# Optimization experiments

Measured on AMD Instinct MI355X. Metric: run time of the kernel, lower is better.

## Reference

```python
import jax, jax.numpy as jnp
import numpy as np

B, IN_DIM, HIDDEN, OUT_DIM = 256, 100000, 512, 30000
KS, DIM = 256, 2
S = HIDDEN // DIM  # number of PQ subspaces = 256


def setup_inputs() -> dict:
    key = jax.random.key(0)
    ks = jax.random.split(key, 6)
    x = jax.random.uniform(ks[0], (B, IN_DIM), dtype=jnp.float32)
    w1 = jax.random.normal(ks[1], (HIDDEN, IN_DIM), dtype=jnp.float32) * 0.01
    b1 = jax.random.normal(ks[2], (HIDDEN,), dtype=jnp.float32)
    codebooks = jax.random.normal(ks[3], (S, KS, DIM), dtype=jnp.float32) * 0.05
    codes = jax.random.randint(ks[4], (OUT_DIM, S), 0, KS, dtype=jnp.int64)
    b2 = jax.random.normal(ks[5], (OUT_DIM,), dtype=jnp.float32) * 0.01
    return {"x": x, "w1": w1, "b1": b1, "codebooks": codebooks,
            "codes": codes, "b2": b2}


def reference(x, w1, b1, codebooks, codes, b2):
    # fc1: SparseLinear == x @ w1.T + b1 (spmm with dense math)
    h = jax.nn.relu(jnp.einsum('bi,hi->bh', x, w1) + b1)  # [B, HIDDEN]
    # fc2: VQLinear -- reconstruct PQ weight via codebook gather
    # codebooks: [S, KS, DIM], codes: [OUT_DIM, S] -> w2: [OUT_DIM, S, DIM]
    w2 = codebooks[jnp.arange(S)[None, :], codes]            # gather per subspace
    w2 = w2.reshape(OUT_DIM, HIDDEN)                         # [OUT_DIM, HIDDEN]
    logits = jnp.einsum('bh,oh->bo', h, w2) + b2             # [B, OUT_DIM]
    # original applies log_softmax over dim=0 (batch axis)
    return jax.nn.log_softmax(logits, axis=0)
```

## Files before the change

### kernel.cpp

```cpp
#include <hip/hip_runtime.h>
#include <cstdint>
#include <cstddef>

#define B_ 256
#define IN_ 100000
#define H_ 512
#define OUT_ 30000
#define OUTP_ 30080
#define S_ 256
#define NSTEPS 3125
#define KSPLIT 64

typedef __attribute__((ext_vector_type(4))) float f32x4;
typedef __attribute__((ext_vector_type(2))) float f32x2;
typedef __attribute__((ext_vector_type(4))) int i32x4;
typedef __attribute__((ext_vector_type(8))) short short8;
typedef __attribute__((ext_vector_type(8))) unsigned short ushort8;
typedef __attribute__((ext_vector_type(4))) unsigned short ushort4_;
typedef __attribute__((ext_vector_type(2))) uint32_t uint32x2;
typedef __attribute__((ext_vector_type(4))) uint32_t uint32x4;

static __device__ __forceinline__ uint32_t cvtpk(float lo, float hi) {
  uint32_t r;
  asm("v_cvt_pk_bf16_f32 %0, %1, %2" : "=v"(r) : "v"(lo), "v"(hi));
  return r;
}
static __device__ __forceinline__ unsigned short f2bf(float f) {
  union { float f; uint32_t u; } c; c.f = f;
  uint32_t u = c.u;
  u += 0x7FFFu + ((u >> 16) & 1u);
  return (unsigned short)(u >> 16);
}
static __device__ __forceinline__ float bf2f(unsigned short h) {
  union { uint32_t u; float f; } c; c.u = ((uint32_t)h) << 16;
  return c.f;
}
static __device__ __forceinline__ void pack4_store(unsigned short* dst, f32x4 a) {
  uint32x2 v;
  v[0] = cvtpk(a[0], a[1]); v[1] = cvtpk(a[2], a[3]);
  *(uint32x2*)dst = v;
}

#define BARRIER() { asm volatile("s_waitcnt lgkmcnt(0)" ::: "memory"); \
    __builtin_amdgcn_s_barrier(); \
    __builtin_amdgcn_sched_barrier(0); }

__global__ __launch_bounds__(512, 2) void k_gemm1(const float* __restrict__ x,
                                                  const float* __restrict__ w1,
                                                  unsigned short* __restrict__ part) {
  __shared__ alignas(16) unsigned short Ab[2][B_ * 32];
  __shared__ alignas(16) unsigned short Bb[2][128 * 32];
  const int tid = threadIdx.x;
  const int d = blockIdx.x;
  const int xcd = d & 7;
  const int i = d >> 3;
  const int kc = xcd + ((i >> 2) << 3);
  const int nblk = i & 3;
  const int s0 = (kc * NSTEPS) / KSPLIT;
  const int s1 = ((kc + 1) * NSTEPS) / KSPLIT;
  const int U = s1 - s0;

  const int arow = tid >> 3;
  const int asl = tid & 7;
  const size_t rowStride64 = (size_t)64 * IN_;
  const float* gA = x + (size_t)arow * IN_ + (size_t)s0 * 32 + asl * 4;
  const int afz = (arow >> 1) & 3;
  const int aslSw = ((asl >> 1) ^ afz) * 8 + (asl & 1) * 4;

  const int br = tid >> 3;
  const int bj = tid & 7;
  const float* gB = w1 + (size_t)(nblk * 128 + br) * IN_ + (size_t)s0 * 32 + bj * 4;
  const int bOff = br * 32 + (((bj >> 1) ^ ((br >> 1) & 3)) * 8) + (bj & 1) * 4;

  const int lane = tid & 63;
  const int wid = tid >> 6;
  const int wrow = wid >> 1;
  const int wcol = wid & 1;
  const int fr = lane & 15;
  const int fq = lane >> 4;
  const int Ra = wrow * 64 + fr;
  const int Rb = wcol * 64 + fr;
  const int aBase = Ra * 32 + (fq ^ ((Ra >> 1) & 3)) * 8;
  const int bBase = Rb * 32 + (fq ^ ((Rb >> 1) & 3)) * 8;

  f32x4 zero = {0.f, 0.f, 0.f, 0.f};
  f32x4 acc[4][4];
  #pragma unroll
  for (int mf = 0; mf < 4; ++mf)
    #pragma unroll
    for (int nf = 0; nf < 4; ++nf) acc[mf][nf] = zero;

  f32x4 P0, P1, P2, P3, P4, P5;
  f32x4 Q0, Q1, Q2, Q3, Q4, Q5;
  f32x4 R0, R1, R2, R3, R4, R5;
  f32x4 S0, S1, S2, S3, S4, S5;

#define G1_ISSUE(S, u) if ((u) < U) { \
    const float* pa_ = gA + (size_t)(u) * 32; \
    S##0 = *(const f32x4*)pa_; \
    S##1 = *(const f32x4*)(pa_ + rowStride64); \
    S##2 = *(const f32x4*)(pa_ + 2 * rowStride64); \
    S##3 = *(const f32x4*)(pa_ + 3 * rowStride64); \
    const float* pb_ = gB + (size_t)(u) * 32; \
    S##4 = *(const f32x4*)pb_; \
    S##5 = *(const f32x4*)(pb_ + rowStride64); }

#define G1_PACK(S, b) { \
    pack4_store(&Ab[b][(arow)       * 32 + aslSw], S##0); \
    pack4_store(&Ab[b][(arow + 64)  * 32 + aslSw], S##1); \
    pack4_store(&Ab[b][(arow + 128) * 32 + aslSw], S##2); \
    pack4_store(&Ab[b][(arow + 192) * 32 + aslSw], S##3); \
    pack4_store(&Bb[b][bOff], S##4); \
    pack4_store(&Bb[b][bOff + 64 * 32], S##5); }

#define COMPUTE_TILE(b) { \
    short8 af_[4], bf_[4]; \
    _Pragma("unroll") for (int mf_ = 0; mf_ < 4; ++mf_) af_[mf_] = *(const short8*)&Ab[b][aBase + mf_ * 512]; \
    _Pragma("unroll") for (int nf_ = 0; nf_ < 4; ++nf_) bf_[nf_] = *(const short8*)&Bb[b][bBase + nf_ * 512]; \
    __builtin_amdgcn_s_setprio(1); \
    _Pragma("unroll") for (int mf_ = 0; mf_ < 4; ++mf_) \
      _Pragma("unroll") for (int nf_ = 0; nf_ < 4; ++nf_) \
        acc[mf_][nf_] = __builtin_amdgcn_mfma_f32_16x16x32_bf16(af_[mf_], bf_[nf_], acc[mf_][nf_], 0, 0, 0); \
    __builtin_amdgcn_s_setprio(0); }

  G1_ISSUE(P, 0)
  G1_ISSUE(Q, 1)
  G1_ISSUE(R, 2)
  G1_ISSUE(S, 3)
  G1_PACK(P, 0)
  BARRIER()

  int u = 0;
  #pragma unroll 1
  while (u + 3 < U) {
    G1_ISSUE(P, u + 4)
    COMPUTE_TILE(0)
    G1_PACK(Q, 1)
    BARRIER()
    G1_ISSUE(Q, u + 5)
    COMPUTE_TILE(1)
    G1_PACK(R, 0)
    BARRIER()
    G1_ISSUE(R, u + 6)
    COMPUTE_TILE(0)
    G1_PACK(S, 1)
    BARRIER()
    G1_ISSUE(S, u + 7)
    COMPUTE_TILE(1)
    if (u + 4 < U) { G1_PACK(P, 0) }
    BARRIER()
    u += 4;
  }
  if (u < U)     COMPUTE_TILE(0)
  if (u + 1 < U) { G1_PACK(Q, 1) BARRIER() COMPUTE_TILE(1) }
  if (u + 2 < U) { G1_PACK(R, 0) BARRIER() COMPUTE_TILE(0) }
  if (u + 3 < U) { G1_PACK(S, 1) BARRIER() COMPUTE_TILE(1) }

  unsigned short* pp = part + (size_t)kc * (B_ * H_);
  #pragma unroll
  for (int mf = 0; mf < 4; ++mf) {
    #pragma unroll
    for (int nf = 0; nf < 4; ++nf) {
      const int row0 = wrow * 64 + mf * 16 + fq * 4;
      const int col = nblk * 128 + wcol * 64 + nf * 16 + fr;
      #pragma unroll
      for (int j = 0; j < 4; ++j)
        pp[(size_t)(row0 + j) * H_ + col] = f2bf(acc[mf][nf][j]);
    }
  }
}

__global__ void k_reduce_h(const unsigned short* __restrict__ part,
                           const float* __restrict__ b1,
                           unsigned short* __restrict__ hbf) {
  int t = blockIdx.x * 256 + threadIdx.x;
  int base = t * 4;
  int n = base & (H_ - 1);
  float a0 = b1[n], a1 = b1[n + 1], a2 = b1[n + 2], a3 = b1[n + 3];
  #pragma unroll 8
  for (int kc = 0; kc < KSPLIT; ++kc) {
    ushort4_ v = *(const ushort4_*)(part + (size_t)kc * (B_ * H_) + base);
    a0 += bf2f(v[0]); a1 += bf2f(v[1]); a2 += bf2f(v[2]); a3 += bf2f(v[3]);
  }
  ushort4_ o;
  o[0] = f2bf(fmaxf(a0, 0.f));
  o[1] = f2bf(fmaxf(a1, 0.f));
  o[2] = f2bf(fmaxf(a2, 0.f));
  o[3] = f2bf(fmaxf(a3, 0.f));
  *(ushort4_*)(hbf + base) = o;
}

__global__ __launch_bounds__(512, 2) void k_gemm2(const unsigned short* __restrict__ hbf,
                                                  const int* __restrict__ codes,
                                                  const float* __restrict__ cb,
                                                  const float* __restrict__ b2,
                                                  float* __restrict__ out) {
  __shared__ alignas(16) unsigned short Ab[2][B_ * 32];
  __shared__ alignas(16) unsigned short Bb[2][128 * 32];
  __shared__ float sred[4][128];
  const int tid = threadIdx.x;
  const int n0 = blockIdx.x * 128;

  const int arow2 = tid >> 2;
  const int asl2 = tid & 3;
  const unsigned short* gA = hbf + (size_t)arow2 * H_ + asl2 * 8;
  const int afz2 = (arow2 >> 1) & 3;
  const int aslSw2 = (asl2 ^ afz2) * 8;
  const int aOffA = arow2 * 32 + aslSw2;
  const int aOffB = (arow2 + 128) * 32 + aslSw2;

  const int rb = tid >> 2;
  const int s4 = tid & 3;
  const int rbo = (n0 + rb < OUT_) ? (n0 + rb) : (OUT_ - 1);
  const int* gC = codes + (size_t)rbo * S_ + s4 * 4;
  const int bOff = rb * 32 + (s4 ^ ((rb >> 1) & 3)) * 8;

  const int lane = tid & 63;
  const int wid = tid >> 6;
  const int wrow = wid >> 1;
  const int wcol = wid & 1;
  const int fr = lane & 15;
  const int fq = lane >> 4;
  const int Ra = wrow * 64 + fr;
  const int Rb = wcol * 64 + fr;
  const int aBase = Ra * 32 + (fq ^ ((Ra >> 1) & 3)) * 8;
  const int bBase = Rb * 32 + (fq ^ ((Rb >> 1) & 3)) * 8;

  f32x4 zero = {0.f, 0.f, 0.f, 0.f};
  f32x4 acc[4][4];
  #pragma unroll
  for (int mf = 0; mf < 4; ++mf)
    #pragma unroll
    for (int nf = 0; nf < 4; ++nf) acc[mf][nf] = zero;

  ushort8 Pa0, Pa1, Qa0, Qa1;
  i32x4 Pc, Qc;
  f32x2 Pg0, Pg1, Pg2, Pg3, Qg0, Qg1, Qg2, Qg3;

#define G2_IC(S, u) if ((u) < 16) { \
    S##a0 = *(const ushort8*)(gA + (size_t)(u) * 32); \
    S##a1 = *(const ushort8*)(gA + (size_t)(u) * 32 + (size_t)128 * H_); \
    S##c  = *(const i32x4*)(gC + (u) * 16); }

#define G2_IG(S, u) if ((u) < 16) { \
    const int slb_ = (u) * 16 + s4 * 4; \
    S##g0 = *(const f32x2*)(cb + ((size_t)(slb_ + 0) * 256 + (S##c[0] & 255)) * 2); \
    S##g1 = *(const f32x2*)(cb + ((size_t)(slb_ + 1) * 256 + (S##c[1] & 255)) * 2); \
    S##g2 = *(const f32x2*)(cb + ((size_t)(slb_ + 2) * 256 + (S##c[2] & 255)) * 2); \
    S##g3 = *(const f32x2*)(cb + ((size_t)(slb_ + 3) * 256 + (S##c[3] & 255)) * 2); }

#define G2_PACK(S, b) { \
    *(ushort8*)&Ab[b][aOffA] = S##a0; \
    *(ushort8*)&Ab[b][aOffB] = S##a1; \
    uint32x4 bw_; \
    bw_[0] = cvtpk(S##g0[0], S##g0[1]); bw_[1] = cvtpk(S##g1[0], S##g1[1]); \
    bw_[2] = cvtpk(S##g2[0], S##g2[1]); bw_[3] = cvtpk(S##g3[0], S##g3[1]); \
    *(uint32x4*)&Bb[b][bOff] = bw_; }

#define G2_COMPUTE(b) { \
    short8 af_[4], bf_[4]; \
    _Pragma("unroll") for (int mf_ = 0; mf_ < 4; ++mf_) af_[mf_] = *(const short8*)&Ab[b][aBase + mf_ * 512]; \
    _Pragma("unroll") for (int nf_ = 0; nf_ < 4; ++nf_) bf_[nf_] = *(const short8*)&Bb[b][bBase + nf_ * 512]; \
    __builtin_amdgcn_s_setprio(1); \
    _Pragma("unroll") for (int mf_ = 0; mf_ < 4; ++mf_) \
      _Pragma("unroll") for (int nf_ = 0; nf_ < 4; ++nf_) \
        acc[mf_][nf_] = __builtin_amdgcn_mfma_f32_16x16x32_bf16(af_[mf_], bf_[nf_], acc[mf_][nf_], 0, 0, 0); \
    __builtin_amdgcn_s_setprio(0); }

  G2_IC(P, 0)
  G2_IC(Q, 1)
  G2_IG(P, 0)
  G2_PACK(P, 0)
  BARRIER()

  #pragma unroll 1
  for (int u = 0; u < 16; u += 2) {
    G2_IC(P, u + 2)
    G2_IG(Q, u + 1)
    G2_COMPUTE(0)
    G2_PACK(Q, 1)
    BARRIER()
    G2_IC(Q, u + 3)
    G2_IG(P, u + 2)
    G2_COMPUTE(1)
    if (u + 2 < 16) { G2_PACK(P, 0) }
    BARRIER()
  }

  float b2v[4];
  #pragma unroll
  for (int nf = 0; nf < 4; ++nf) {
    int col = n0 + wcol * 64 + nf * 16 + fr;
    b2v[nf] = (col < OUT_) ? b2[col] : 0.f;
  }
  #pragma unroll
  for (int mf = 0; mf < 4; ++mf)
    #pragma unroll
    for (int nf = 0; nf < 4; ++nf)
      #pragma unroll
      for (int j = 0; j < 4; ++j) acc[mf][nf][j] += b2v[nf];

  float cmax[4];
  #pragma unroll
  for (int nf = 0; nf < 4; ++nf) {
    float m = -3.4e38f;
    #pragma unroll
    for (int mf = 0; mf < 4; ++mf)
      #pragma unroll
      for (int j = 0; j < 4; ++j) m = fmaxf(m, acc[mf][nf][j]);
    m = fmaxf(m, __shfl_xor(m, 16, 64));
    m = fmaxf(m, __shfl_xor(m, 32, 64));
    cmax[nf] = m;
  }
  if (lane < 16) {
    #pragma unroll
    for (int nf = 0; nf < 4; ++nf) sred[wrow][wcol * 64 + nf * 16 + lane] = cmax[nf];
  }
  __syncthreads();
  float cm[4];
  #pragma unroll
  for (int nf = 0; nf < 4; ++nf) {
    int ci = wcol * 64 + nf * 16 + fr;
    cm[nf] = fmaxf(fmaxf(sred[0][ci], sred[1][ci]), fmaxf(sred[2][ci], sred[3][ci]));
  }
  __syncthreads();

  float cs[4];
  #pragma unroll
  for (int nf = 0; nf < 4; ++nf) {
    float sum = 0.f;
    #pragma unroll
    for (int mf = 0; mf < 4; ++mf)
      #pragma unroll
      for (int j = 0; j < 4; ++j) sum += expf(acc[mf][nf][j] - cm[nf]);
    sum += __shfl_xor(sum, 16, 64);
    sum += __shfl_xor(sum, 32, 64);
    cs[nf] = sum;
  }
  if (lane < 16) {
    #pragma unroll
    for (int nf = 0; nf < 4; ++nf) sred[wrow][wcol * 64 + nf * 16 + lane] = cs[nf];
  }
  __syncthreads();
  float lden[4];
  #pragma unroll
  for (int nf = 0; nf < 4; ++nf) {
    int ci = wcol * 64 + nf * 16 + fr;
    lden[nf] = logf(sred[0][ci] + sred[1][ci] + sred[2][ci] + sred[3][ci]);
  }

  #pragma unroll
  for (int mf = 0; mf < 4; ++mf) {
    #pragma unroll
    for (int nf = 0; nf < 4; ++nf) {
      int col = n0 + wcol * 64 + nf * 16 + fr;
      if (col < OUT_) {
        int row0 = wrow * 64 + mf * 16 + fq * 4;
        #pragma unroll
        for (int j = 0; j < 4; ++j)
          out[(size_t)(row0 + j) * OUT_ + col] = acc[mf][nf][j] - cm[nf] - lden[nf];
      }
    }
  }
}

extern "C" void kernel_launch(void* const* d_in, const int* in_sizes, int n_in,
                              void* d_out, int out_size, void* d_ws, size_t ws_size,
                              hipStream_t stream) {
  const float* x      = (const float*)d_in[0];
  const float* w1     = (const float*)d_in[1];
  const float* b1     = (const float*)d_in[2];
  const float* cb     = (const float*)d_in[3];
  const int*   codes  = (const int*)d_in[4];
  const float* b2     = (const float*)d_in[5];
  float* out = (float*)d_out;

  char* ws = (char*)d_ws;
  unsigned short* part = (unsigned short*)ws;
  unsigned short* hbf  = (unsigned short*)(ws + (size_t)KSPLIT * B_ * H_ * 2);

  hipLaunchKernelGGL(k_gemm1,    dim3(4 * KSPLIT),          dim3(512), 0, stream, x, w1, part);
  hipLaunchKernelGGL(k_reduce_h, dim3((B_ * H_ / 4) / 256), dim3(256), 0, stream, part, b1, hbf);
  hipLaunchKernelGGL(k_gemm2,    dim3(OUTP_ / 128),         dim3(512), 0, stream, hbf, codes, cb, b2, out);
}
```

Before: 120.4 us.

## Stream fp32 tiles directly into LDS via global_load_lds triple buffering

Replaces the register-staged load, bf16 pack and LDS store pipeline in the first GEMM with direct global-to-LDS DMA (global_load_lds, 16 bytes per lane) into a three-stage fp32 LDS ring. The bf16 conversion moves to the LDS read side just before the MFMAs. The aim is to free VGPRs and VALU work from staging and to overlap loads with compute using a vmcnt-based wait. In exchange LDS footprint doubles per stage (fp32, three buffers, about 144KB), which may limit occupancy at two blocks per CU, and each tile now needs twice the LDS read traffic plus conversion work per compute step.

```diff
diff --git a/kernel.cpp b/kernel.cpp
--- a/kernel.cpp
+++ b/kernel.cpp
@@ -20,6 +20,8 @@
 typedef __attribute__((ext_vector_type(2))) uint32_t uint32x2;
 typedef __attribute__((ext_vector_type(4))) uint32_t uint32x4;
 
+union U32S8 { uint32x4 u; short8 s; };
+
 static __device__ __forceinline__ uint32_t cvtpk(float lo, float hi) {
   uint32_t r;
   asm("v_cvt_pk_bf16_f32 %0, %1, %2" : "=v"(r) : "v"(lo), "v"(hi));
@@ -35,21 +37,25 @@
   union { uint32_t u; float f; } c; c.u = ((uint32_t)h) << 16;
   return c.f;
 }
-static __device__ __forceinline__ void pack4_store(unsigned short* dst, f32x4 a) {
-  uint32x2 v;
-  v[0] = cvtpk(a[0], a[1]); v[1] = cvtpk(a[2], a[3]);
-  *(uint32x2*)dst = v;
+
+static __device__ __forceinline__ void gload_lds16(const float* g, float* l) {
+  __builtin_amdgcn_global_load_lds((const __attribute__((address_space(1))) void*)g,
+                                   (__attribute__((address_space(3))) void*)l, 16, 0, 0);
 }
 
 #define BARRIER() { asm volatile("s_waitcnt lgkmcnt(0)" ::: "memory"); \
     __builtin_amdgcn_s_barrier(); \
     __builtin_amdgcn_sched_barrier(0); }
 
+#define WAITBAR() { asm volatile("s_waitcnt vmcnt(6) lgkmcnt(0)" ::: "memory"); \
+    __builtin_amdgcn_s_barrier(); \
+    __builtin_amdgcn_sched_barrier(0); }
+
 __global__ __launch_bounds__(512, 2) void k_gemm1(const float* __restrict__ x,
                                                   const float* __restrict__ w1,
                                                   unsigned short* __restrict__ part) {
-  __shared__ alignas(16) unsigned short Ab[2][B_ * 32];
-  __shared__ alignas(16) unsigned short Bb[2][128 * 32];
+  __shared__ alignas(16) float Af32[3][B_ * 32];
+  __shared__ alignas(16) float Bf32[3][128 * 32];
   const int tid = threadIdx.x;
   const int d = blockIdx.x;
   const int xcd = d & 7;
@@ -60,28 +66,22 @@
   const int s1 = ((kc + 1) * NSTEPS) / KSPLIT;
   const int U = s1 - s0;
 
-  const int arow = tid >> 3;
-  const int asl = tid & 7;
-  const size_t rowStride64 = (size_t)64 * IN_;
-  const float* gA = x + (size_t)arow * IN_ + (size_t)s0 * 32 + asl * 4;
-  const int afz = (arow >> 1) & 3;
-  const int aslSw = ((asl >> 1) ^ afz) * 8 + (asl & 1) * 4;
-
-  const int br = tid >> 3;
-  const int bj = tid & 7;
-  const float* gB = w1 + (size_t)(nblk * 128 + br) * IN_ + (size_t)s0 * 32 + bj * 4;
-  const int bOff = br * 32 + (((bj >> 1) ^ ((br >> 1) & 3)) * 8) + (bj & 1) * 4;
-
   const int lane = tid & 63;
   const int wid = tid >> 6;
+
+  const int drow = lane >> 3;
+  const int lc = (lane & 7) ^ drow;
+  const float* gAd = x + (size_t)(32 * wid + drow) * IN_ + (size_t)s0 * 32 + lc * 4;
+  const float* gBd = w1 + (size_t)(nblk * 128 + 16 * wid + drow) * IN_ + (size_t)s0 * 32 + lc * 4;
+  const int ldsA = wid * 1024;
+  const int ldsB = wid * 512;
+
   const int wrow = wid >> 1;
   const int wcol = wid & 1;
   const int fr = lane & 15;
   const int fq = lane >> 4;
-  const int Ra = wrow * 64 + fr;
-  const int Rb = wcol * 64 + fr;
-  const int aBase = Ra * 32 + (fq ^ ((Ra >> 1) & 3)) * 8;
-  const int bBase = Rb * 32 + (fq ^ ((Rb >> 1) & 3)) * 8;
+  const int aOffF = (wrow * 64 + fr) * 32 + ((2 * fq) ^ (fr & 7)) * 4;
+  const int bOffF = (wcol * 64 + fr) * 32 + ((2 * fq) ^ (fr & 7)) * 4;
 
   f32x4 zero = {0.f, 0.f, 0.f, 0.f};
   f32x4 acc[4][4];
@@ -90,71 +90,57 @@
     #pragma unroll
     for (int nf = 0; nf < 4; ++nf) acc[mf][nf] = zero;
 
-  f32x4 P0, P1, P2, P3, P4, P5;
-  f32x4 Q0, Q1, Q2, Q3, Q4, Q5;
-  f32x4 R0, R1, R2, R3, R4, R5;
-  f32x4 S0, S1, S2, S3, S4, S5;
-
-#define G1_ISSUE(S, u) if ((u) < U) { \
-    const float* pa_ = gA + (size_t)(u) * 32; \
-    S##0 = *(const f32x4*)pa_; \
-    S##1 = *(const f32x4*)(pa_ + rowStride64); \
-    S##2 = *(const f32x4*)(pa_ + 2 * rowStride64); \
-    S##3 = *(const f32x4*)(pa_ + 3 * rowStride64); \
-    const float* pb_ = gB + (size_t)(u) * 32; \
-    S##4 = *(const f32x4*)pb_; \
-    S##5 = *(const f32x4*)(pb_ + rowStride64); }
-
-#define G1_PACK(S, b) { \
-    pack4_store(&Ab[b][(arow)       * 32 + aslSw], S##0); \
-    pack4_store(&Ab[b][(arow + 64)  * 32 + aslSw], S##1); \
-    pack4_store(&Ab[b][(arow + 128) * 32 + aslSw], S##2); \
-    pack4_store(&Ab[b][(arow + 192) * 32 + aslSw], S##3); \
-    pack4_store(&Bb[b][bOff], S##4); \
-    pack4_store(&Bb[b][bOff + 64 * 32], S##5); }
-
-#define COMPUTE_TILE(b) { \
+#define G1_DMA(v, DB) { \
+    const int vc_ = (v) < U ? (v) : U - 1; \
+    const float* ga_ = gAd + (size_t)vc_ * 32; \
+    const float* gb_ = gBd + (size_t)vc_ * 32; \
+    gload_lds16(ga_,                       &Af32[DB][ldsA]); \
+    gload_lds16(ga_ +  8 * (size_t)IN_,    &Af32[DB][ldsA + 256]); \
+    gload_lds16(ga_ + 16 * (size_t)IN_,    &Af32[DB][ldsA + 512]); \
+    gload_lds16(ga_ + 24 * (size_t)IN_,    &Af32[DB][ldsA + 768]); \
+    gload_lds16(gb_,                       &Bf32[DB][ldsB]); \
+    gload_lds16(gb_ +  8 * (size_t)IN_,    &Bf32[DB][ldsB + 256]); }
+
+#define G1_COMPUTE(CB) { \
     short8 af_[4], bf_[4]; \
-    _Pragma("unroll") for (int mf_ = 0; mf_ < 4; ++mf_) af_[mf_] = *(const short8*)&Ab[b][aBase + mf_ * 512]; \
-    _Pragma("unroll") for (int nf_ = 0; nf_ < 4; ++nf_) bf_[nf_] = *(const short8*)&Bb[b][bBase + nf_ * 512]; \
+    _Pragma("unroll") for (int mf_ = 0; mf_ < 4; ++mf_) { \
+      f32x4 lo_ = *(const f32x4*)&Af32[CB][aOffF + mf_ * 512]; \
+      f32x4 hi_ = *(const f32x4*)&Af32[CB][(aOffF ^ 4) + mf_ * 512]; \
+      U32S8 t_; \
+      t_.u[0] = cvtpk(lo_[0], lo_[1]); t_.u[1] = cvtpk(lo_[2], lo_[3]); \
+      t_.u[2] = cvtpk(hi_[0], hi_[1]); t_.u[3] = cvtpk(hi_[2], hi_[3]); \
+      af_[mf_] = t_.s; } \
+    _Pragma("unroll") for (int nf_ = 0; nf_ < 4; ++nf_) { \
+      f32x4 lo_ = *(const f32x4*)&Bf32[CB][bOffF + nf_ * 512]; \
+      f32x4 hi_ = *(const f32x4*)&Bf32[CB][(bOffF ^ 4) + nf_ * 512]; \
+      U32S8 t_; \
+      t_.u[0] = cvtpk(lo_[0], lo_[1]); t_.u[1] = cvtpk(lo_[2], lo_[3]); \
+      t_.u[2] = cvtpk(hi_[0], hi_[1]); t_.u[3] = cvtpk(hi_[2], hi_[3]); \
+      bf_[nf_] = t_.s; } \
     __builtin_amdgcn_s_setprio(1); \
     _Pragma("unroll") for (int mf_ = 0; mf_ < 4; ++mf_) \
       _Pragma("unroll") for (int nf_ = 0; nf_ < 4; ++nf_) \
         acc[mf_][nf_] = __builtin_amdgcn_mfma_f32_16x16x32_bf16(af_[mf_], bf_[nf_], acc[mf_][nf_], 0, 0, 0); \
     __builtin_amdgcn_s_setprio(0); }
 
-  G1_ISSUE(P, 0)
-  G1_ISSUE(Q, 1)
-  G1_ISSUE(R, 2)
-  G1_ISSUE(S, 3)
-  G1_PACK(P, 0)
-  BARRIER()
+#define G1_ITER(v, CB, DB) { \
+    WAITBAR() \
+    G1_DMA((v) + 2, DB) \
+    G1_COMPUTE(CB) }
+
+  G1_DMA(0, 0)
+  G1_DMA(1, 1)
 
   int u = 0;
   #pragma unroll 1
-  while (u + 3 < U) {
-    G1_ISSUE(P, u + 4)
-    COMPUTE_TILE(0)
-    G1_PACK(Q, 1)
-    BARRIER()
-    G1_ISSUE(Q, u + 5)
-    COMPUTE_TILE(1)
-    G1_PACK(R, 0)
-    BARRIER()
-    G1_ISSUE(R, u + 6)
-    COMPUTE_TILE(0)
-    G1_PACK(S, 1)
-    BARRIER()
-    G1_ISSUE(S, u + 7)
-    COMPUTE_TILE(1)
-    if (u + 4 < U) { G1_PACK(P, 0) }
-    BARRIER()
-    u += 4;
-  }
-  if (u < U)     COMPUTE_TILE(0)
-  if (u + 1 < U) { G1_PACK(Q, 1) BARRIER() COMPUTE_TILE(1) }
-  if (u + 2 < U) { G1_PACK(R, 0) BARRIER() COMPUTE_TILE(0) }
-  if (u + 3 < U) { G1_PACK(S, 1) BARRIER() COMPUTE_TILE(1) }
+  while (u + 2 < U) {
+    G1_ITER(u,     0, 2)
+    G1_ITER(u + 1, 1, 0)
+    G1_ITER(u + 2, 2, 1)
+    u += 3;
+  }
+  if (u < U)     { G1_ITER(u,     0, 2) }
+  if (u + 1 < U) { G1_ITER(u + 1, 1, 0) }
 
   unsigned short* pp = part + (size_t)kc * (B_ * H_);
   #pragma unroll
```

Measured after the change: 132.7 us. 10.2% more time.
